# Optimization experiments

Hardware: AMD Instinct MI355X
Metric: run time of the kernel (lower is better)

The kernel has to match this reference:

```python
import jax, jax.numpy as jnp
import numpy as np

D_MODEL = 1024
NUM_HEADS = 16
D_K = D_MODEL // NUM_HEADS


def setup_inputs() -> dict:
    key = jax.random.key(0)
    ks = jax.random.split(key, 9)
    s = 1.0 / np.sqrt(D_MODEL)
    x = jax.random.normal(ks[0], (4, 2048, D_MODEL), dtype=jnp.float32)
    wq = jax.random.uniform(ks[1], (D_MODEL, D_MODEL), jnp.float32, -s, s)
    bq = jax.random.uniform(ks[2], (D_MODEL,), jnp.float32, -s, s)
    wk = jax.random.uniform(ks[3], (D_MODEL, D_MODEL), jnp.float32, -s, s)
    bk = jax.random.uniform(ks[4], (D_MODEL,), jnp.float32, -s, s)
    wv = jax.random.uniform(ks[5], (D_MODEL, D_MODEL), jnp.float32, -s, s)
    bv = jax.random.uniform(ks[6], (D_MODEL,), jnp.float32, -s, s)
    wo = jax.random.uniform(ks[7], (D_MODEL, D_MODEL), jnp.float32, -s, s)
    bo = jax.random.uniform(ks[8], (D_MODEL,), jnp.float32, -s, s)
    return {"x": x, "wq": wq, "bq": bq, "wk": wk, "bk": bk,
            "wv": wv, "bv": bv, "wo": wo, "bo": bo}


def reference(x, wq, bq, wk, bk, wv, bv, wo, bo):
    B, S, _ = x.shape
    H, Dk = NUM_HEADS, D_K
    # QKV projections (torch Linear: y = x @ W.T + b; here w* stored as [in,out])
    q = (x @ wq + bq).reshape(B, S, H, Dk).transpose(0, 2, 1, 3)  # [B,H,S,Dk]
    k = (x @ wk + bk).reshape(B, S, H, Dk).transpose(0, 2, 1, 3)
    v = (x @ wv + bv).reshape(B, S, H, Dk).transpose(0, 2, 1, 3)
    scores = jnp.einsum('bhqd,bhkd->bhqk', q, k) / jnp.sqrt(jnp.float32(Dk))
    attn = jax.nn.softmax(scores, axis=-1)
    out = jnp.einsum('bhqk,bhkd->bhqd', attn, v)  # [B,H,S,Dk]
    out = out.transpose(0, 2, 1, 3).reshape(B, S, H * Dk)
    return out @ wo + bo
```

## Files before the change

### kernel.cpp

```cpp
#include <hip/hip_runtime.h>
#include <hip/hip_bf16.h>
#include <cstdint>

#define D_MODEL 1024
#define NHEAD 16
#define DKH 64
#define BATCH 4
#define SEQ 2048
#define M_TOT (BATCH*SEQ)

typedef __bf16 bf16;
typedef __bf16 bf16x8 __attribute__((ext_vector_type(8)));
typedef __bf16 bf16x4 __attribute__((ext_vector_type(4)));
typedef float  f32x4  __attribute__((ext_vector_type(4)));

__device__ __forceinline__ void async_ld16(const void* g, void* l) {
    __builtin_amdgcn_global_load_lds(
        (__attribute__((address_space(1))) void*)(uintptr_t)g,
        (__attribute__((address_space(3))) void*)(uintptr_t)l,
        16, 0, 0);
}

__global__ __launch_bounds__(256) void k_cvt_x(const float* __restrict__ x,
                                               bf16* __restrict__ xb) {
    int i = (blockIdx.x * 256 + threadIdx.x) * 4;
    float4 f = *(const float4*)(x + i);
    bf16x4 o;
    o[0] = (bf16)f.x; o[1] = (bf16)f.y; o[2] = (bf16)f.z; o[3] = (bf16)f.w;
    *(bf16x4*)(xb + i) = o;
}

__global__ __launch_bounds__(256) void k_cvt_w(const float* __restrict__ wq,
                                               const float* __restrict__ wk,
                                               const float* __restrict__ wv,
                                               const float* __restrict__ wo,
                                               bf16* __restrict__ wt) {
    int z = blockIdx.z;
    const float* W = (z == 0) ? wq : (z == 1) ? wk : (z == 2) ? wv : wo;
    bf16* T = wt + (size_t)z * D_MODEL * D_MODEL;
    __shared__ float t[32][33];
    int tx = threadIdx.x, ty = threadIdx.y;
    int bx = blockIdx.x * 32, by = blockIdx.y * 32;
#pragma unroll
    for (int i = 0; i < 4; i++)
        t[ty + i * 8][tx] = W[(size_t)(by + ty + i * 8) * D_MODEL + bx + tx];
    __syncthreads();
#pragma unroll
    for (int i = 0; i < 4; i++)
        T[(size_t)(bx + ty + i * 8) * D_MODEL + by + tx] = (bf16)t[tx][ty + i * 8];
}

__global__ __launch_bounds__(256) void k_gemm_qkv(const bf16* __restrict__ xb,
                                                  const bf16* __restrict__ wt,
                                                  const float* __restrict__ bq,
                                                  const float* __restrict__ bk,
                                                  const float* __restrict__ bv,
                                                  bf16* __restrict__ qkv) {
    int z = blockIdx.z;
    const bf16* W = wt + (size_t)z * D_MODEL * D_MODEL;
    const float* bias = (z == 0) ? bq : (z == 1) ? bk : bv;
    bf16* out = qkv + (size_t)z * M_TOT * D_MODEL;
    float scale = (z == 0) ? 0.125f * 1.44269504088896f : 1.0f;

    __shared__ bf16 As[128 * 32];
    __shared__ bf16 Bs[128 * 32];

    int tid = threadIdx.x;
    int lane = tid & 63, wid = tid >> 6;
    int ln = lane & 15, qd = lane >> 4;
    int wm = wid >> 1, wn = wid & 1;
    int m0 = blockIdx.y * 128, n0 = blockIdx.x * 128;

    f32x4 zero4 = {0.f, 0.f, 0.f, 0.f};
    f32x4 acc[4][4];
#pragma unroll
    for (int i = 0; i < 4; i++)
#pragma unroll
        for (int j = 0; j < 4; j++) acc[i][j] = zero4;

    for (int k0 = 0; k0 < D_MODEL; k0 += 32) {
#pragma unroll
        for (int t = 0; t < 2; t++) {
            int c = t * 256 + tid;
            async_ld16(xb + (size_t)(m0 + (c >> 2)) * D_MODEL + k0 + (c & 3) * 8,
                       As + (c & ~63) * 8);
            async_ld16(W + (size_t)(n0 + (c >> 2)) * D_MODEL + k0 + (c & 3) * 8,
                       Bs + (c & ~63) * 8);
        }
        __syncthreads();
        bf16x8 af[4], bfr[4];
#pragma unroll
        for (int mi = 0; mi < 4; mi++)
            af[mi] = *(const bf16x8*)(As + (wm * 64 + mi * 16 + ln) * 32 + qd * 8);
#pragma unroll
        for (int ni = 0; ni < 4; ni++)
            bfr[ni] = *(const bf16x8*)(Bs + (wn * 64 + ni * 16 + ln) * 32 + qd * 8);
#pragma unroll
        for (int mi = 0; mi < 4; mi++)
#pragma unroll
            for (int ni = 0; ni < 4; ni++)
                acc[mi][ni] = __builtin_amdgcn_mfma_f32_16x16x32_bf16(af[mi], bfr[ni],
                                                                      acc[mi][ni], 0, 0, 0);
        __syncthreads();
    }

#pragma unroll
    for (int ni = 0; ni < 4; ni++) {
        int col = n0 + wn * 64 + ni * 16 + ln;
        float bcol = bias[col];
        int h = col >> 6, d = col & 63;
#pragma unroll
        for (int mi = 0; mi < 4; mi++) {
            int rb = m0 + wm * 64 + mi * 16 + qd * 4;
#pragma unroll
            for (int r = 0; r < 4; r++) {
                int row = rb + r;
                int b = row >> 11, s = row & 2047;
                float v = (acc[mi][ni][r] + bcol) * scale;
                out[(((size_t)(b * NHEAD + h)) * SEQ + s) * DKH + d] = (bf16)v;
            }
        }
    }
}

__global__ __launch_bounds__(256) void k_tr_v(const bf16* __restrict__ vg,
                                              bf16* __restrict__ vtg) {
    __shared__ bf16 t[64][65];
    int bh = blockIdx.y;
    int s0 = blockIdx.x * 64;
    int tx = threadIdx.x, ty = threadIdx.y;
#pragma unroll
    for (int i = 0; i < 16; i++)
        t[ty + i * 4][tx] = vg[((size_t)bh * SEQ + s0 + ty + i * 4) * DKH + tx];
    __syncthreads();
#pragma unroll
    for (int i = 0; i < 16; i++)
        vtg[((size_t)bh * DKH + ty + i * 4) * SEQ + s0 + tx] = t[tx][ty + i * 4];
}

#define PROW 40
__global__ __launch_bounds__(256, 4) void k_attn(const bf16* __restrict__ qg,
                                                 const bf16* __restrict__ kg,
                                                 const bf16* __restrict__ vtg,
                                                 bf16* __restrict__ og) {
    __shared__ bf16 Ks[2 * 64 * 32];
    __shared__ bf16 Vs[2 * 64 * 32];
    __shared__ bf16 Ps[4 * 2 * 32 * PROW];

    int tid = threadIdx.x;
    int lane = tid & 63, wid = tid >> 6;
    int ln = lane & 15, qd = lane >> 4;
    int bh = blockIdx.y;
    int q0 = blockIdx.x * 128;
    int b = bh >> 4, h = bh & 15;

    const bf16* qp = qg + (size_t)bh * SEQ * DKH;
    const bf16* kp = kg + (size_t)bh * SEQ * DKH;
    const bf16* vp = vtg + (size_t)bh * DKH * SEQ;

    bf16x8 qa[2][2];
#pragma unroll
    for (int mi = 0; mi < 2; mi++)
#pragma unroll
        for (int kc = 0; kc < 2; kc++)
            qa[mi][kc] = *(const bf16x8*)(qp + (size_t)(q0 + wid * 32 + mi * 16 + ln) * DKH
                                          + kc * 32 + qd * 8);

    bf16 onev = (bf16)((ln == 0) ? 1.0f : 0.0f);
    bf16x8 ones_frag = {onev, onev, onev, onev, onev, onev, onev, onev};

    f32x4 zero4 = {0.f, 0.f, 0.f, 0.f};
    f32x4 o_acc[2][4];
    f32x4 l_acc[2];
#pragma unroll
    for (int mi = 0; mi < 2; mi++) {
        l_acc[mi] = zero4;
#pragma unroll
        for (int nd = 0; nd < 4; nd++) o_acc[mi][nd] = zero4;
    }

    bf16* Pw = Ps + wid * 2 * 32 * PROW;

    for (int kt = 0; kt < SEQ; kt += 64) {
#pragma unroll
        for (int t = 0; t < 2; t++) {
            int c = t * 256 + tid;
            int ch = c >> 8, w = c & 255;
            int row = w >> 2, part = w & 3;
            async_ld16(kp + (size_t)(kt + row) * DKH + ch * 32 + part * 8,
                       Ks + (c & ~63) * 8);
            async_ld16(vp + (size_t)row * SEQ + kt + ch * 32 + part * 8,
                       Vs + (c & ~63) * 8);
        }
        __syncthreads();

        f32x4 sc[2][4];
#pragma unroll
        for (int mi = 0; mi < 2; mi++)
#pragma unroll
            for (int ni = 0; ni < 4; ni++) sc[mi][ni] = zero4;
#pragma unroll
        for (int kc = 0; kc < 2; kc++) {
#pragma unroll
            for (int ni = 0; ni < 4; ni++) {
                bf16x8 kb = *(const bf16x8*)(Ks + kc * 2048 + (ni * 16 + ln) * 32 + qd * 8);
#pragma unroll
                for (int mi = 0; mi < 2; mi++)
                    sc[mi][ni] = __builtin_amdgcn_mfma_f32_16x16x32_bf16(kb, qa[mi][kc],
                                                                         sc[mi][ni], 0, 0, 0);
            }
        }

#pragma unroll
        for (int mi = 0; mi < 2; mi++) {
#pragma unroll
            for (int ni = 0; ni < 4; ni++) {
                bf16x4 p4;
#pragma unroll
                for (int r = 0; r < 4; r++)
                    p4[r] = (bf16)__builtin_amdgcn_exp2f(sc[mi][ni][r]);
                *(bf16x4*)(Pw + (ni >> 1) * 32 * PROW + (mi * 16 + ln) * PROW
                           + (ni & 1) * 16 + qd * 4) = p4;
            }
        }

#pragma unroll
        for (int kc2 = 0; kc2 < 2; kc2++) {
            bf16x8 pf[2];
#pragma unroll
            for (int mi = 0; mi < 2; mi++) {
                pf[mi] = *(const bf16x8*)(Pw + kc2 * 32 * PROW + (mi * 16 + ln) * PROW + qd * 8);
                l_acc[mi] = __builtin_amdgcn_mfma_f32_16x16x32_bf16(pf[mi], ones_frag,
                                                                    l_acc[mi], 0, 0, 0);
            }
#pragma unroll
            for (int nd = 0; nd < 4; nd++) {
                bf16x8 vf = *(const bf16x8*)(Vs + kc2 * 2048 + (nd * 16 + ln) * 32 + qd * 8);
#pragma unroll
                for (int mi = 0; mi < 2; mi++)
                    o_acc[mi][nd] = __builtin_amdgcn_mfma_f32_16x16x32_bf16(pf[mi], vf,
                                                                            o_acc[mi][nd], 0, 0, 0);
            }
        }
        __syncthreads();
    }

#pragma unroll
    for (int mi = 0; mi < 2; mi++) {
#pragma unroll
        for (int r = 0; r < 4; r++) {
            float lsum = __shfl(l_acc[mi][r], lane & 48, 64);
            float inv = 1.0f / lsum;
            int s = q0 + wid * 32 + mi * 16 + qd * 4 + r;
            size_t rowoff = ((size_t)b * SEQ + s) * D_MODEL + h * DKH;
#pragma unroll
            for (int nd = 0; nd < 4; nd++)
                og[rowoff + nd * 16 + ln] = (bf16)(o_acc[mi][nd][r] * inv);
        }
    }
}

__global__ __launch_bounds__(256) void k_gemm_out(const bf16* __restrict__ ob,
                                                  const bf16* __restrict__ wot,
                                                  const float* __restrict__ bo,
                                                  float* __restrict__ out) {
    __shared__ bf16 As[128 * 32];
    __shared__ bf16 Bs[128 * 32];

    int tid = threadIdx.x;
    int lane = tid & 63, wid = tid >> 6;
    int ln = lane & 15, qd = lane >> 4;
    int wm = wid >> 1, wn = wid & 1;
    int m0 = blockIdx.y * 128, n0 = blockIdx.x * 128;

    f32x4 zero4 = {0.f, 0.f, 0.f, 0.f};
    f32x4 acc[4][4];
#pragma unroll
    for (int i = 0; i < 4; i++)
#pragma unroll
        for (int j = 0; j < 4; j++) acc[i][j] = zero4;

    for (int k0 = 0; k0 < D_MODEL; k0 += 32) {
#pragma unroll
        for (int t = 0; t < 2; t++) {
            int c = t * 256 + tid;
            async_ld16(ob + (size_t)(m0 + (c >> 2)) * D_MODEL + k0 + (c & 3) * 8,
                       As + (c & ~63) * 8);
            async_ld16(wot + (size_t)(n0 + (c >> 2)) * D_MODEL + k0 + (c & 3) * 8,
                       Bs + (c & ~63) * 8);
        }
        __syncthreads();
        bf16x8 af[4], bfr[4];
#pragma unroll
        for (int mi = 0; mi < 4; mi++)
            af[mi] = *(const bf16x8*)(As + (wm * 64 + mi * 16 + ln) * 32 + qd * 8);
#pragma unroll
        for (int ni = 0; ni < 4; ni++)
            bfr[ni] = *(const bf16x8*)(Bs + (wn * 64 + ni * 16 + ln) * 32 + qd * 8);
#pragma unroll
        for (int mi = 0; mi < 4; mi++)
#pragma unroll
            for (int ni = 0; ni < 4; ni++)
                acc[mi][ni] = __builtin_amdgcn_mfma_f32_16x16x32_bf16(af[mi], bfr[ni],
                                                                      acc[mi][ni], 0, 0, 0);
        __syncthreads();
    }

#pragma unroll
    for (int ni = 0; ni < 4; ni++) {
        int col = n0 + wn * 64 + ni * 16 + ln;
        float bcol = bo[col];
#pragma unroll
        for (int mi = 0; mi < 4; mi++) {
            int rb = m0 + wm * 64 + mi * 16 + qd * 4;
#pragma unroll
            for (int r = 0; r < 4; r++) {
                int row = rb + r;
                out[(size_t)row * D_MODEL + col] = acc[mi][ni][r] + bcol;
            }
        }
    }
}

extern "C" void kernel_launch(void* const* d_in, const int* in_sizes, int n_in,
                              void* d_out, int out_size, void* d_ws, size_t ws_size,
                              hipStream_t stream) {
    const float* x  = (const float*)d_in[0];
    const float* wq = (const float*)d_in[1];
    const float* bq = (const float*)d_in[2];
    const float* wk = (const float*)d_in[3];
    const float* bk = (const float*)d_in[4];
    const float* wv = (const float*)d_in[5];
    const float* bv = (const float*)d_in[6];
    const float* wo = (const float*)d_in[7];
    const float* bo = (const float*)d_in[8];
    float* out = (float*)d_out;

    char* ws = (char*)d_ws;
    bf16* xb  = (bf16*)ws;
    bf16* wt  = (bf16*)(ws + 16777216);
    bf16* qkv = (bf16*)(ws + 25165824);
    bf16* vtg = (bf16*)(ws + 75497472);
    bf16* og  = xb;

    k_cvt_x<<<dim3(8192), dim3(256), 0, stream>>>(x, xb);
    k_cvt_w<<<dim3(32, 32, 4), dim3(32, 8), 0, stream>>>(wq, wk, wv, wo, wt);
    k_gemm_qkv<<<dim3(8, 64, 3), dim3(256), 0, stream>>>(xb, wt, bq, bk, bv, qkv);
    k_tr_v<<<dim3(32, 64), dim3(64, 4), 0, stream>>>(qkv + 2 * (size_t)M_TOT * D_MODEL, vtg);
    k_attn<<<dim3(16, 64), dim3(256), 0, stream>>>(qkv, qkv + (size_t)M_TOT * D_MODEL, vtg, og);
    k_gemm_out<<<dim3(8, 64), dim3(256), 0, stream>>>(og, wt + 3 * (size_t)D_MODEL * D_MODEL,
                                                      bo, out);
}
```

Baseline: 297.2 us.

## Fuse conversion kernels, write V transposed from QKV GEMM, vectorize epilogues

Merges the x and weight conversion kernels into one launch. The QKV GEMM epilogue now writes V directly in transposed layout, which removes the separate V-transpose kernel and its extra pass over memory. For Q/K and the output GEMM, the MFMA operands are swapped so each lane holds four consecutive columns, which allows packed 4-wide stores and vector bias loads. The cost is a branch on z inside the GEMM and strided 8-byte stores for the transposed V.

```diff
diff --git a/kernel.cpp b/kernel.cpp
--- a/kernel.cpp
+++ b/kernel.cpp
@@ -21,33 +21,37 @@
         16, 0, 0);
 }
 
-__global__ __launch_bounds__(256) void k_cvt_x(const float* __restrict__ x,
-                                               bf16* __restrict__ xb) {
-    int i = (blockIdx.x * 256 + threadIdx.x) * 4;
-    float4 f = *(const float4*)(x + i);
-    bf16x4 o;
-    o[0] = (bf16)f.x; o[1] = (bf16)f.y; o[2] = (bf16)f.z; o[3] = (bf16)f.w;
-    *(bf16x4*)(xb + i) = o;
-}
-
-__global__ __launch_bounds__(256) void k_cvt_w(const float* __restrict__ wq,
-                                               const float* __restrict__ wk,
-                                               const float* __restrict__ wv,
-                                               const float* __restrict__ wo,
-                                               bf16* __restrict__ wt) {
-    int z = blockIdx.z;
-    const float* W = (z == 0) ? wq : (z == 1) ? wk : (z == 2) ? wv : wo;
-    bf16* T = wt + (size_t)z * D_MODEL * D_MODEL;
+__global__ __launch_bounds__(256) void k_cvt(const float* __restrict__ x,
+                                             bf16* __restrict__ xb,
+                                             const float* __restrict__ wq,
+                                             const float* __restrict__ wk,
+                                             const float* __restrict__ wv,
+                                             const float* __restrict__ wo,
+                                             bf16* __restrict__ wt) {
     __shared__ float t[32][33];
-    int tx = threadIdx.x, ty = threadIdx.y;
-    int bx = blockIdx.x * 32, by = blockIdx.y * 32;
-#pragma unroll
-    for (int i = 0; i < 4; i++)
-        t[ty + i * 8][tx] = W[(size_t)(by + ty + i * 8) * D_MODEL + bx + tx];
-    __syncthreads();
-#pragma unroll
-    for (int i = 0; i < 4; i++)
-        T[(size_t)(bx + ty + i * 8) * D_MODEL + by + tx] = (bf16)t[tx][ty + i * 8];
+    int bid = blockIdx.x;
+    if (bid < 8192) {
+        int i = (bid * 256 + threadIdx.x) * 4;
+        float4 f = *(const float4*)(x + i);
+        bf16x4 o;
+        o[0] = (bf16)f.x; o[1] = (bf16)f.y; o[2] = (bf16)f.z; o[3] = (bf16)f.w;
+        *(bf16x4*)(xb + i) = o;
+    } else {
+        int wb = bid - 8192;
+        int z = wb >> 10;
+        int rem = wb & 1023;
+        const float* W = (z == 0) ? wq : (z == 1) ? wk : (z == 2) ? wv : wo;
+        bf16* T = wt + (size_t)z * D_MODEL * D_MODEL;
+        int tx = threadIdx.x & 31, ty = threadIdx.x >> 5;
+        int bx = (rem & 31) * 32, by = (rem >> 5) * 32;
+#pragma unroll
+        for (int i = 0; i < 4; i++)
+            t[ty + i * 8][tx] = W[(size_t)(by + ty + i * 8) * D_MODEL + bx + tx];
+        __syncthreads();
+#pragma unroll
+        for (int i = 0; i < 4; i++)
+            T[(size_t)(bx + ty + i * 8) * D_MODEL + by + tx] = (bf16)t[tx][ty + i * 8];
+    }
 }
 
 __global__ __launch_bounds__(256) void k_gemm_qkv(const bf16* __restrict__ xb,
@@ -55,11 +59,11 @@
                                                   const float* __restrict__ bq,
                                                   const float* __restrict__ bk,
                                                   const float* __restrict__ bv,
-                                                  bf16* __restrict__ qkv) {
+                                                  bf16* __restrict__ qkv,
+                                                  bf16* __restrict__ vtg) {
     int z = blockIdx.z;
     const bf16* W = wt + (size_t)z * D_MODEL * D_MODEL;
     const float* bias = (z == 0) ? bq : (z == 1) ? bk : bv;
-    bf16* out = qkv + (size_t)z * M_TOT * D_MODEL;
     float scale = (z == 0) ? 0.125f * 1.44269504088896f : 1.0f;
 
     __shared__ bf16 As[128 * 32];
@@ -78,6 +82,7 @@
 #pragma unroll
         for (int j = 0; j < 4; j++) acc[i][j] = zero4;
 
+    bool swapped = (z < 2);
     for (int k0 = 0; k0 < D_MODEL; k0 += 32) {
 #pragma unroll
         for (int t = 0; t < 2; t++) {
@@ -95,47 +100,60 @@
 #pragma unroll
         for (int ni = 0; ni < 4; ni++)
             bfr[ni] = *(const bf16x8*)(Bs + (wn * 64 + ni * 16 + ln) * 32 + qd * 8);
-#pragma unroll
-        for (int mi = 0; mi < 4; mi++)
-#pragma unroll
-            for (int ni = 0; ni < 4; ni++)
-                acc[mi][ni] = __builtin_amdgcn_mfma_f32_16x16x32_bf16(af[mi], bfr[ni],
-                                                                      acc[mi][ni], 0, 0, 0);
-        __syncthreads();
-    }
-
-#pragma unroll
-    for (int ni = 0; ni < 4; ni++) {
-        int col = n0 + wn * 64 + ni * 16 + ln;
-        float bcol = bias[col];
-        int h = col >> 6, d = col & 63;
+        if (swapped) {
+#pragma unroll
+            for (int mi = 0; mi < 4; mi++)
+#pragma unroll
+                for (int ni = 0; ni < 4; ni++)
+                    acc[mi][ni] = __builtin_amdgcn_mfma_f32_16x16x32_bf16(bfr[ni], af[mi],
+                                                                          acc[mi][ni], 0, 0, 0);
+        } else {
+#pragma unroll
+            for (int mi = 0; mi < 4; mi++)
+#pragma unroll
+                for (int ni = 0; ni < 4; ni++)
+                    acc[mi][ni] = __builtin_amdgcn_mfma_f32_16x16x32_bf16(af[mi], bfr[ni],
+                                                                          acc[mi][ni], 0, 0, 0);
+        }
+        __syncthreads();
+    }
+
+    if (swapped) {
+        bf16* out = qkv + (size_t)z * M_TOT * D_MODEL;
 #pragma unroll
         for (int mi = 0; mi < 4; mi++) {
-            int rb = m0 + wm * 64 + mi * 16 + qd * 4;
-#pragma unroll
-            for (int r = 0; r < 4; r++) {
-                int row = rb + r;
-                int b = row >> 11, s = row & 2047;
-                float v = (acc[mi][ni][r] + bcol) * scale;
-                out[(((size_t)(b * NHEAD + h)) * SEQ + s) * DKH + d] = (bf16)v;
-            }
-        }
-    }
-}
-
-__global__ __launch_bounds__(256) void k_tr_v(const bf16* __restrict__ vg,
-                                              bf16* __restrict__ vtg) {
-    __shared__ bf16 t[64][65];
-    int bh = blockIdx.y;
-    int s0 = blockIdx.x * 64;
-    int tx = threadIdx.x, ty = threadIdx.y;
-#pragma unroll
-    for (int i = 0; i < 16; i++)
-        t[ty + i * 4][tx] = vg[((size_t)bh * SEQ + s0 + ty + i * 4) * DKH + tx];
-    __syncthreads();
-#pragma unroll
-    for (int i = 0; i < 16; i++)
-        vtg[((size_t)bh * DKH + ty + i * 4) * SEQ + s0 + tx] = t[tx][ty + i * 4];
+            int srow = m0 + wm * 64 + mi * 16 + ln;
+            int b = srow >> 11, s = srow & 2047;
+#pragma unroll
+            for (int ni = 0; ni < 4; ni++) {
+                int col4 = n0 + wn * 64 + ni * 16 + qd * 4;
+                f32x4 bb = *(const f32x4*)(bias + col4);
+                int h = col4 >> 6, d = col4 & 63;
+                bf16x4 p;
+#pragma unroll
+                for (int r = 0; r < 4; r++)
+                    p[r] = (bf16)((acc[mi][ni][r] + bb[r]) * scale);
+                *(bf16x4*)(out + (((size_t)(b * NHEAD + h)) * SEQ + s) * DKH + d) = p;
+            }
+        }
+    } else {
+#pragma unroll
+        for (int ni = 0; ni < 4; ni++) {
+            int col = n0 + wn * 64 + ni * 16 + ln;
+            float bcol = bias[col];
+            int h = col >> 6, d = col & 63;
+#pragma unroll
+            for (int mi = 0; mi < 4; mi++) {
+                int rb = m0 + wm * 64 + mi * 16 + qd * 4;
+                int b = rb >> 11, s = rb & 2047;
+                bf16x4 p;
+#pragma unroll
+                for (int r = 0; r < 4; r++)
+                    p[r] = (bf16)(acc[mi][ni][r] + bcol);
+                *(bf16x4*)(vtg + (((size_t)(b * NHEAD + h)) * DKH + d) * SEQ + s) = p;
+            }
+        }
+    }
 }
 
 #define PROW 40
@@ -301,23 +319,22 @@
         for (int mi = 0; mi < 4; mi++)
 #pragma unroll
             for (int ni = 0; ni < 4; ni++)
-                acc[mi][ni] = __builtin_amdgcn_mfma_f32_16x16x32_bf16(af[mi], bfr[ni],
+                acc[mi][ni] = __builtin_amdgcn_mfma_f32_16x16x32_bf16(bfr[ni], af[mi],
                                                                       acc[mi][ni], 0, 0, 0);
         __syncthreads();
     }
 
 #pragma unroll
-    for (int ni = 0; ni < 4; ni++) {
-        int col = n0 + wn * 64 + ni * 16 + ln;
-        float bcol = bo[col];
-#pragma unroll
-        for (int mi = 0; mi < 4; mi++) {
-            int rb = m0 + wm * 64 + mi * 16 + qd * 4;
-#pragma unroll
-            for (int r = 0; r < 4; r++) {
-                int row = rb + r;
-                out[(size_t)row * D_MODEL + col] = acc[mi][ni][r] + bcol;
-            }
+    for (int mi = 0; mi < 4; mi++) {
+        int row = m0 + wm * 64 + mi * 16 + ln;
+#pragma unroll
+        for (int ni = 0; ni < 4; ni++) {
+            int col4 = n0 + wn * 64 + ni * 16 + qd * 4;
+            f32x4 bb = *(const f32x4*)(bo + col4);
+            f32x4 v;
+#pragma unroll
+            for (int r = 0; r < 4; r++) v[r] = acc[mi][ni][r] + bb[r];
+            *(f32x4*)(out + (size_t)row * D_MODEL + col4) = v;
         }
     }
 }
@@ -343,10 +360,8 @@
     bf16* vtg = (bf16*)(ws + 75497472);
     bf16* og  = xb;
 
-    k_cvt_x<<<dim3(8192), dim3(256), 0, stream>>>(x, xb);
-    k_cvt_w<<<dim3(32, 32, 4), dim3(32, 8), 0, stream>>>(wq, wk, wv, wo, wt);
-    k_gemm_qkv<<<dim3(8, 64, 3), dim3(256), 0, stream>>>(xb, wt, bq, bk, bv, qkv);
-    k_tr_v<<<dim3(32, 64), dim3(64, 4), 0, stream>>>(qkv + 2 * (size_t)M_TOT * D_MODEL, vtg);
+    k_cvt<<<dim3(8192 + 4096), dim3(256), 0, stream>>>(x, xb, wq, wk, wv, wo, wt);
+    k_gemm_qkv<<<dim3(8, 64, 3), dim3(256), 0, stream>>>(xb, wt, bq, bk, bv, qkv, vtg);
     k_attn<<<dim3(16, 64), dim3(256), 0, stream>>>(qkv, qkv + (size_t)M_TOT * D_MODEL, vtg, og);
     k_gemm_out<<<dim3(8, 64), dim3(256), 0, stream>>>(og, wt + 3 * (size_t)D_MODEL * D_MODEL,
                                                       bo, out);
```

After: 294.7 us. Within noise of the previous version (-0.8%).
